# Kernel tuning notes

Hardware: AMD Instinct MI355X
Metric: run time of the kernel (lower is better)

The kernel has to match this reference:

```python
import jax, jax.numpy as jnp
import numpy as np

FEATURES = 768

def setup_inputs() -> dict:
    key = jax.random.key(0)
    k1, k2, kq, kd, kc = jax.random.split(key, 5)
    B, S1, S2 = 8, 2048, 2048
    bound = 1.0 / np.sqrt(FEATURES)  # nn.Linear default init range
    return {
        "matrix1": jax.random.normal(k1, (B, S1, FEATURES), dtype=jnp.float32),
        "matrix2": jax.random.normal(k2, (B, S2, FEATURES), dtype=jnp.float32),
        "w_q": jax.random.uniform(kq, (FEATURES,), jnp.float32, -bound, bound),
        "w_d": jax.random.uniform(kd, (FEATURES,), jnp.float32, -bound, bound),
        "w_c": jax.random.uniform(kc, (FEATURES,), jnp.float32, -bound, bound),
    }

def reference(matrix1, matrix2, w_q, w_d, w_c):
    # S[b,j,k] = (m1 @ w_q)[b,j] + (m2 @ w_d)[b,k] + sum_f w_c[f]*m1[b,j,f]*m2[b,k,f]
    Q = jnp.einsum('bjf,f->bj', matrix1, w_q)                # [B, S1]
    D = jnp.einsum('bkf,f->bk', matrix2, w_d)                # [B, S2]
    C = jnp.einsum('bjf,bkf->bjk', matrix1 * w_c, matrix2)   # [B, S1, S2]
    return Q[:, :, None] + D[:, None, :] + C
```

## Files before the change

kernel.cpp:

```cpp
#include <hip/hip_runtime.h>
#include <hip/hip_bf16.h>

#define S1 2048
#define S2 2048
#define FEAT 768
#define NB 8
#define BK 64
#define NKT (FEAT / BK)

typedef __attribute__((ext_vector_type(8))) short bf16x8;
typedef __attribute__((ext_vector_type(4))) float f32x4;
typedef __attribute__((ext_vector_type(4))) unsigned short us4;
typedef __attribute__((address_space(1))) const unsigned int gu32;
typedef __attribute__((address_space(3))) unsigned int lu32;

static __device__ __forceinline__ unsigned short f2bf(float x) {
    unsigned u = __builtin_bit_cast(unsigned, x);
    unsigned r = u + 0x7FFFu + ((u >> 16) & 1u);
    return (unsigned short)(r >> 16);
}

__global__ __launch_bounds__(256) void conv_kernel(
    const float* __restrict__ m1, const float* __restrict__ m2,
    const float* __restrict__ wq, const float* __restrict__ wd,
    const float* __restrict__ wc,
    unsigned short* __restrict__ A, unsigned short* __restrict__ Bm,
    float* __restrict__ Q, float* __restrict__ D) {
    int wave = threadIdx.x >> 6;
    int lane = threadIdx.x & 63;
    int g = blockIdx.x * 4 + wave;
    bool isA = (g < NB * S1);
    int row = isA ? g : g - NB * S1;
    const float* src = isA ? m1 : m2;
    const float* w   = isA ? wq : wd;
    unsigned short* dst = (isA ? A : Bm) + (size_t)row * FEAT;
    const float4* rp = (const float4*)(src + (size_t)row * FEAT);
    const float4* wp = (const float4*)w;
    const float4* cp = (const float4*)wc;
    float acc = 0.f;
#pragma unroll
    for (int i = 0; i < 3; ++i) {
        int idx = lane + 64 * i;
        float4 a = rp[idx];
        float4 b = wp[idx];
        acc += a.x * b.x + a.y * b.y + a.z * b.z + a.w * b.w;
        float4 c;
        if (isA) c = cp[idx]; else c = float4{1.f, 1.f, 1.f, 1.f};
        us4 v = { f2bf(a.x * c.x), f2bf(a.y * c.y),
                  f2bf(a.z * c.z), f2bf(a.w * c.w) };
        *(us4*)(dst + idx * 4) = v;
    }
#pragma unroll
    for (int s = 32; s; s >>= 1) acc += __shfl_xor(acc, s, 64);
    if (lane == 0) (isA ? Q : D)[row] = acc;
}

__global__ __launch_bounds__(256, 3) void gemm128_kernel(
    const unsigned short* __restrict__ A, const unsigned short* __restrict__ Bm,
    const float* __restrict__ Q, const float* __restrict__ D,
    float* __restrict__ out) {

    __shared__ __align__(16) char sA[128 * 128];
    __shared__ __align__(16) char sB[128 * 128];

    const int bid = blockIdx.x;
    const int b   = bid & 7;
    const int idx = bid >> 3;
    const int qd  = idx >> 6;
    const int w64 = idx & 63;
    const int tm  = ((qd >> 1) << 3) | (w64 >> 3);
    const int tn  = ((qd & 1) << 3) | (w64 & 7);

    const int tid  = threadIdx.x;
    const int lane = tid & 63;
    const int wave = tid >> 6;
    const int wm = wave >> 1, wn = wave & 1;

    const char* Ab = (const char*)(A + ((size_t)b * S1 + (size_t)tm * 128) * FEAT);
    const char* Bb = (const char*)(Bm + ((size_t)b * S2 + (size_t)tn * 128) * FEAT);

    const int srow = lane >> 3;
    const int scol = ((lane & 7) ^ (srow & 7)) * 16;

    const int fr = lane & 15;
    const int kg = lane >> 4;

    f32x4 acc[4][4];
#pragma unroll
    for (int m = 0; m < 4; ++m)
#pragma unroll
        for (int n = 0; n < 4; ++n) acc[m][n] = (f32x4)0.f;

    for (int kt = 0; kt < NKT; ++kt) {
        __syncthreads();
#pragma unroll
        for (int i = 0; i < 4; ++i) {
            const int rb = wave * 32 + i * 8;
            __builtin_amdgcn_global_load_lds(
                (gu32*)(Ab + (size_t)(rb + srow) * (FEAT * 2) + kt * (BK * 2) + scol),
                (lu32*)(sA + rb * 128), 16, 0, 0);
            __builtin_amdgcn_global_load_lds(
                (gu32*)(Bb + (size_t)(rb + srow) * (FEAT * 2) + kt * (BK * 2) + scol),
                (lu32*)(sB + rb * 128), 16, 0, 0);
        }
        __syncthreads();

#pragma unroll
        for (int s = 0; s < 2; ++s) {
            bf16x8 af[4], bfr[4];
#pragma unroll
            for (int m = 0; m < 4; ++m) {
                int r = wm * 64 + m * 16 + fr;
                int coff = (s * 64 + kg * 16) ^ ((r & 7) << 4);
                af[m] = *(const bf16x8*)(sA + r * 128 + coff);
            }
#pragma unroll
            for (int n = 0; n < 4; ++n) {
                int r = wn * 64 + n * 16 + fr;
                int coff = (s * 64 + kg * 16) ^ ((r & 7) << 4);
                bfr[n] = *(const bf16x8*)(sB + r * 128 + coff);
            }
#pragma unroll
            for (int m = 0; m < 4; ++m)
#pragma unroll
                for (int n = 0; n < 4; ++n)
                    acc[m][n] = __builtin_amdgcn_mfma_f32_16x16x32_bf16(
                        af[m], bfr[n], acc[m][n], 0, 0, 0);
        }
    }

    const float* Qb = Q + b * S1 + tm * 128;
    const float* Db = D + b * S2 + tn * 128;
    float dv[4];
#pragma unroll
    for (int n = 0; n < 4; ++n) dv[n] = Db[wn * 64 + n * 16 + fr];

    const size_t outbase = ((size_t)b * S1 + (size_t)tm * 128) * S2 + (size_t)tn * 128;
#pragma unroll
    for (int m = 0; m < 4; ++m) {
#pragma unroll
        for (int i = 0; i < 4; ++i) {
            int rl = wm * 64 + m * 16 + kg * 4 + i;
            float qv = Qb[rl];
            float* orow = out + outbase + (size_t)rl * S2 + wn * 64;
#pragma unroll
            for (int n = 0; n < 4; ++n)
                orow[n * 16 + fr] = acc[m][n][i] + qv + dv[n];
        }
    }
}

__global__ __launch_bounds__(256) void qd_kernel(
    const float* __restrict__ m1, const float* __restrict__ m2,
    const float* __restrict__ wq, const float* __restrict__ wd,
    float* __restrict__ Q, float* __restrict__ D) {
    int wave = threadIdx.x >> 6;
    int lane = threadIdx.x & 63;
    int g = blockIdx.x * 4 + wave;
    const float* src; const float* w; float* dst; int row;
    if (g < NB * S1) { src = m1; w = wq; dst = Q; row = g; }
    else             { src = m2; w = wd; dst = D; row = g - NB * S1; }
    const float4* rp = (const float4*)(src + (size_t)row * FEAT);
    const float4* wp = (const float4*)w;
    float acc = 0.f;
#pragma unroll
    for (int i = 0; i < 3; ++i) {
        float4 a = rp[lane + 64 * i];
        float4 b = wp[lane + 64 * i];
        acc += a.x * b.x + a.y * b.y + a.z * b.z + a.w * b.w;
    }
#pragma unroll
    for (int s = 32; s; s >>= 1) acc += __shfl_xor(acc, s, 64);
    if (lane == 0) dst[row] = acc;
}

__global__ __launch_bounds__(256) void gemm_kernel(
    const float* __restrict__ m1, const float* __restrict__ m2,
    const float* __restrict__ wc,
    const float* __restrict__ Q, const float* __restrict__ D,
    float* __restrict__ out) {

    __shared__ __align__(16) char sA[128 * 64 * 2];
    __shared__ __align__(16) char sB[128 * 64 * 2];
    __shared__ float wcs[FEAT];

    const int tid = threadIdx.x;
    const int blk = blockIdx.x;
    const int b  = blk >> 8;
    const int t  = blk & 255;
    const int tm = t >> 4, tn = t & 15;

    for (int i = tid; i < FEAT; i += 256) wcs[i] = wc[i];

    const float* Abase = m1 + ((size_t)b * S1 + (size_t)tm * 128) * FEAT;
    const float* Bbase = m2 + ((size_t)b * S2 + (size_t)tn * 128) * FEAT;

    const int lane = tid & 63;
    const int wave = tid >> 6;
    const int wm = wave >> 1, wn = wave & 1;

    f32x4 acc[4][4];
#pragma unroll
    for (int m = 0; m < 4; ++m)
#pragma unroll
        for (int n = 0; n < 4; ++n) acc[m][n] = (f32x4)0.f;

    const int col4 = tid & 15;
    const int row0 = tid >> 4;

    __syncthreads();

    for (int ks = 0; ks < FEAT / 64; ++ks) {
        float4 wc4 = *(const float4*)&wcs[ks * 64 + col4 * 4];
        const float4* Ak = (const float4*)(Abase + ks * 64);
        const float4* Bk = (const float4*)(Bbase + ks * 64);

        __syncthreads();
#pragma unroll
        for (int i = 0; i < 8; ++i) {
            int r = row0 + 16 * i;
            float4 a = Ak[(size_t)r * (FEAT / 4) + col4];
            us4 av = { f2bf(a.x * wc4.x), f2bf(a.y * wc4.y),
                       f2bf(a.z * wc4.z), f2bf(a.w * wc4.w) };
            int off = r * 128 + ((col4 * 8) ^ ((r & 7) << 4));
            *(us4*)(sA + off) = av;
        }
#pragma unroll
        for (int i = 0; i < 8; ++i) {
            int r = row0 + 16 * i;
            float4 v = Bk[(size_t)r * (FEAT / 4) + col4];
            us4 bv = { f2bf(v.x), f2bf(v.y), f2bf(v.z), f2bf(v.w) };
            int off = r * 128 + ((col4 * 8) ^ ((r & 7) << 4));
            *(us4*)(sB + off) = bv;
        }
        __syncthreads();

#pragma unroll
        for (int s = 0; s < 2; ++s) {
            bf16x8 af[4], bfr[4];
#pragma unroll
            for (int m = 0; m < 4; ++m) {
                int r = wm * 64 + m * 16 + (lane & 15);
                int coff = (s * 64 + (lane >> 4) * 16) ^ ((r & 7) << 4);
                af[m] = *(const bf16x8*)(sA + r * 128 + coff);
            }
#pragma unroll
            for (int n = 0; n < 4; ++n) {
                int r = wn * 64 + n * 16 + (lane & 15);
                int coff = (s * 64 + (lane >> 4) * 16) ^ ((r & 7) << 4);
                bfr[n] = *(const bf16x8*)(sB + r * 128 + coff);
            }
#pragma unroll
            for (int m = 0; m < 4; ++m)
#pragma unroll
                for (int n = 0; n < 4; ++n)
                    acc[m][n] = __builtin_amdgcn_mfma_f32_16x16x32_bf16(
                        af[m], bfr[n], acc[m][n], 0, 0, 0);
        }
    }

    const float* Qb = Q + b * S1 + tm * 128;
    const float* Db = D + b * S2 + tn * 128;
    float dv[4];
#pragma unroll
    for (int n = 0; n < 4; ++n) dv[n] = Db[wn * 64 + n * 16 + (lane & 15)];

    const size_t outbase = ((size_t)b * S1 + (size_t)tm * 128) * S2 + (size_t)tn * 128;
#pragma unroll
    for (int m = 0; m < 4; ++m) {
#pragma unroll
        for (int i = 0; i < 4; ++i) {
            int rl = wm * 64 + m * 16 + (lane >> 4) * 4 + i;
            float qv = Qb[rl];
            float* orow = out + outbase + (size_t)rl * S2 + wn * 64;
#pragma unroll
            for (int n = 0; n < 4; ++n) {
                int cl = n * 16 + (lane & 15);
                orow[cl] = acc[m][n][i] + qv + dv[n];
            }
        }
    }
}

extern "C" void kernel_launch(void* const* d_in, const int* in_sizes, int n_in,
                              void* d_out, int out_size, void* d_ws, size_t ws_size,
                              hipStream_t stream) {
    const float* m1 = (const float*)d_in[0];
    const float* m2 = (const float*)d_in[1];
    const float* wq = (const float*)d_in[2];
    const float* wd = (const float*)d_in[3];
    const float* wc = (const float*)d_in[4];
    float* out = (float*)d_out;

    const size_t elems = (size_t)NB * S1 * FEAT;
    const size_t need = 2 * elems * sizeof(unsigned short)
                      + (size_t)(NB * S1 + NB * S2) * sizeof(float);

    if (ws_size >= need) {
        unsigned short* Abuf = (unsigned short*)d_ws;
        unsigned short* Bbuf = Abuf + elems;
        float* Q  = (float*)(Bbuf + elems);
        float* Dv = Q + NB * S1;
        conv_kernel<<<(NB * S1 + NB * S2) / 4, 256, 0, stream>>>(
            m1, m2, wq, wd, wc, Abuf, Bbuf, Q, Dv);
        gemm128_kernel<<<NB * 16 * 16, 256, 0, stream>>>(Abuf, Bbuf, Q, Dv, out);
    } else {
        float* Q  = (float*)d_ws;
        float* Dv = Q + NB * S1;
        qd_kernel<<<(2 * NB * S1) / 4, 256, 0, stream>>>(m1, m2, wq, wd, Q, Dv);
        gemm_kernel<<<NB * 256, 256, 0, stream>>>(m1, m2, wc, Q, Dv, out);
    }
}
```

Measured before the change: 88.30 us.

## Double-buffer LDS tiles with BK=32 to overlap global loads with MFMA

Reworks the bf16 GEMM main loop to use two LDS buffers with half-width K tiles. The next tile is prefetched via global_load_lds while MFMAs run on the current one, and the two barriers per iteration become a single waitcnt plus barrier. The LDS swizzle is changed to match the 64-byte row stride, and the occupancy hint rises from 3 to 4 blocks. The cost is twice as many loop iterations with less MFMA work between barriers.

```diff
diff --git a/kernel.cpp b/kernel.cpp
--- a/kernel.cpp
+++ b/kernel.cpp
@@ -5,7 +5,7 @@
 #define S2 2048
 #define FEAT 768
 #define NB 8
-#define BK 64
+#define BK 32
 #define NKT (FEAT / BK)
 
 typedef __attribute__((ext_vector_type(8))) short bf16x8;
@@ -55,13 +55,12 @@
     if (lane == 0) (isA ? Q : D)[row] = acc;
 }
 
-__global__ __launch_bounds__(256, 3) void gemm128_kernel(
+__global__ __launch_bounds__(256, 4) void gemm128p_kernel(
     const unsigned short* __restrict__ A, const unsigned short* __restrict__ Bm,
     const float* __restrict__ Q, const float* __restrict__ D,
     float* __restrict__ out) {
 
-    __shared__ __align__(16) char sA[128 * 128];
-    __shared__ __align__(16) char sB[128 * 128];
+    __shared__ __align__(16) char ldsb[2 * 16384];
 
     const int bid = blockIdx.x;
     const int b   = bid & 7;
@@ -79,56 +78,70 @@
     const char* Ab = (const char*)(A + ((size_t)b * S1 + (size_t)tm * 128) * FEAT);
     const char* Bb = (const char*)(Bm + ((size_t)b * S2 + (size_t)tn * 128) * FEAT);
 
-    const int srow = lane >> 3;
-    const int scol = ((lane & 7) ^ (srow & 7)) * 16;
-
-    const int fr = lane & 15;
+    const int srow   = lane >> 2;
+    const int scolsw = (((lane & 3) ^ ((lane >> 3) & 3)) * 16);
+
+    const int fr  = lane & 15;
+    const int fkb = (((lane >> 4) ^ ((lane >> 1) & 3)) * 16);
+
+    f32x4 acc[4][4];
+#pragma unroll
+    for (int m = 0; m < 4; ++m)
+#pragma unroll
+        for (int n = 0; n < 4; ++n) acc[m][n] = (f32x4)0.f;
+
+#define STAGE(kt) do {                                                            \
+    char* _buf = ldsb + ((kt) & 1) * 16384;                                       \
+    _Pragma("unroll")                                                             \
+    for (int _i = 0; _i < 2; ++_i) {                                              \
+        const int _j = wave * 2 + _i;            \
+        __builtin_amdgcn_global_load_lds(                                         \
+            (gu32*)(Ab + (size_t)(_j * 16 + srow) * (FEAT * 2)                    \
+                       + (kt) * (BK * 2) + scolsw),                               \
+            (lu32*)(_buf + _j * 1024), 16, 0, 0);                                 \
+        __builtin_amdgcn_global_load_lds(                                         \
+            (gu32*)(Bb + (size_t)(_j * 16 + srow) * (FEAT * 2)                    \
+                       + (kt) * (BK * 2) + scolsw),                               \
+            (lu32*)(_buf + 8192 + _j * 1024), 16, 0, 0);                          \
+    }                                                                             \
+} while (0)
+
+    STAGE(0);
+    asm volatile("s_waitcnt vmcnt(0)" ::: "memory");
+    __builtin_amdgcn_s_barrier();
+    asm volatile("" ::: "memory");
+
+#pragma unroll 2
+    for (int kt = 0; kt < NKT; ++kt) {
+        if (kt + 1 < NKT) STAGE(kt + 1);
+
+        const char* bufc = ldsb + (kt & 1) * 16384;
+        bf16x8 af[4], bfr[4];
+#pragma unroll
+        for (int n = 0; n < 4; ++n) {
+            int r = wn * 64 + n * 16 + fr;
+            bfr[n] = *(const bf16x8*)(bufc + 8192 + r * 64 + fkb);
+        }
+#pragma unroll
+        for (int m = 0; m < 4; ++m) {
+            int r = wm * 64 + m * 16 + fr;
+            af[m] = *(const bf16x8*)(bufc + r * 64 + fkb);
+        }
+#pragma unroll
+        for (int m = 0; m < 4; ++m)
+#pragma unroll
+            for (int n = 0; n < 4; ++n)
+                acc[m][n] = __builtin_amdgcn_mfma_f32_16x16x32_bf16(
+                    af[m], bfr[n], acc[m][n], 0, 0, 0);
+
+        if (kt + 1 < NKT) {
+            asm volatile("s_waitcnt vmcnt(0)" ::: "memory");
+            __builtin_amdgcn_s_barrier();
+            asm volatile("" ::: "memory");
+        }
+    }
+
     const int kg = lane >> 4;
-
-    f32x4 acc[4][4];
-#pragma unroll
-    for (int m = 0; m < 4; ++m)
-#pragma unroll
-        for (int n = 0; n < 4; ++n) acc[m][n] = (f32x4)0.f;
-
-    for (int kt = 0; kt < NKT; ++kt) {
-        __syncthreads();
-#pragma unroll
-        for (int i = 0; i < 4; ++i) {
-            const int rb = wave * 32 + i * 8;
-            __builtin_amdgcn_global_load_lds(
-                (gu32*)(Ab + (size_t)(rb + srow) * (FEAT * 2) + kt * (BK * 2) + scol),
-                (lu32*)(sA + rb * 128), 16, 0, 0);
-            __builtin_amdgcn_global_load_lds(
-                (gu32*)(Bb + (size_t)(rb + srow) * (FEAT * 2) + kt * (BK * 2) + scol),
-                (lu32*)(sB + rb * 128), 16, 0, 0);
-        }
-        __syncthreads();
-
-#pragma unroll
-        for (int s = 0; s < 2; ++s) {
-            bf16x8 af[4], bfr[4];
-#pragma unroll
-            for (int m = 0; m < 4; ++m) {
-                int r = wm * 64 + m * 16 + fr;
-                int coff = (s * 64 + kg * 16) ^ ((r & 7) << 4);
-                af[m] = *(const bf16x8*)(sA + r * 128 + coff);
-            }
-#pragma unroll
-            for (int n = 0; n < 4; ++n) {
-                int r = wn * 64 + n * 16 + fr;
-                int coff = (s * 64 + kg * 16) ^ ((r & 7) << 4);
-                bfr[n] = *(const bf16x8*)(sB + r * 128 + coff);
-            }
-#pragma unroll
-            for (int m = 0; m < 4; ++m)
-#pragma unroll
-                for (int n = 0; n < 4; ++n)
-                    acc[m][n] = __builtin_amdgcn_mfma_f32_16x16x32_bf16(
-                        af[m], bfr[n], acc[m][n], 0, 0, 0);
-        }
-    }
-
     const float* Qb = Q + b * S1 + tm * 128;
     const float* Db = D + b * S2 + tn * 128;
     float dv[4];
@@ -148,6 +161,7 @@
                 orow[n * 16 + fr] = acc[m][n][i] + qv + dv[n];
         }
     }
+#undef STAGE
 }
 
 __global__ __launch_bounds__(256) void qd_kernel(
@@ -303,7 +317,7 @@
         float* Dv = Q + NB * S1;
         conv_kernel<<<(NB * S1 + NB * S2) / 4, 256, 0, stream>>>(
             m1, m2, wq, wd, wc, Abuf, Bbuf, Q, Dv);
-        gemm128_kernel<<<NB * 16 * 16, 256, 0, stream>>>(Abuf, Bbuf, Q, Dv, out);
+        gemm128p_kernel<<<NB * 16 * 16, 256, 0, stream>>>(Abuf, Bbuf, Q, Dv, out);
     } else {
         float* Q  = (float*)d_ws;
         float* Dv = Q + NB * S1;
```

Measured after the change: 98.47 us. 11.5% more time.

## Load GEMM fragments directly from global memory instead of LDS staging

Applied to the files above, without the earlier changes.

The bf16 GEMM no longer stages A and B tiles through shared memory with barriers. Each wave reads its MFMA operand fragments straight from global memory in a fully unrolled K loop, and occupancy is raised to 4 blocks per CU. This removes LDS traffic and __syncthreads overhead. In exchange it relies on L1/L2 caching for operand reuse across waves and issues strided 16-byte global loads.

```diff
diff --git a/kernel.cpp b/kernel.cpp
--- a/kernel.cpp
+++ b/kernel.cpp
@@ -5,14 +5,12 @@
 #define S2 2048
 #define FEAT 768
 #define NB 8
-#define BK 64
+#define BK 32
 #define NKT (FEAT / BK)
 
 typedef __attribute__((ext_vector_type(8))) short bf16x8;
 typedef __attribute__((ext_vector_type(4))) float f32x4;
 typedef __attribute__((ext_vector_type(4))) unsigned short us4;
-typedef __attribute__((address_space(1))) const unsigned int gu32;
-typedef __attribute__((address_space(3))) unsigned int lu32;
 
 static __device__ __forceinline__ unsigned short f2bf(float x) {
     unsigned u = __builtin_bit_cast(unsigned, x);
@@ -55,13 +53,10 @@
     if (lane == 0) (isA ? Q : D)[row] = acc;
 }
 
-__global__ __launch_bounds__(256, 3) void gemm128_kernel(
+__global__ __launch_bounds__(256, 4) void gemm128g_kernel(
     const unsigned short* __restrict__ A, const unsigned short* __restrict__ Bm,
     const float* __restrict__ Q, const float* __restrict__ D,
     float* __restrict__ out) {
-
-    __shared__ __align__(16) char sA[128 * 128];
-    __shared__ __align__(16) char sB[128 * 128];
 
     const int bid = blockIdx.x;
     const int b   = bid & 7;
@@ -76,57 +71,35 @@
     const int wave = tid >> 6;
     const int wm = wave >> 1, wn = wave & 1;
 
-    const char* Ab = (const char*)(A + ((size_t)b * S1 + (size_t)tm * 128) * FEAT);
-    const char* Bb = (const char*)(Bm + ((size_t)b * S2 + (size_t)tn * 128) * FEAT);
-
-    const int srow = lane >> 3;
-    const int scol = ((lane & 7) ^ (srow & 7)) * 16;
-
     const int fr = lane & 15;
     const int kg = lane >> 4;
 
+    const char* Arow = (const char*)(A + ((size_t)b * S1 + (size_t)tm * 128
+                                          + wm * 64 + fr) * FEAT) + kg * 16;
+    const char* Brow = (const char*)(Bm + ((size_t)b * S2 + (size_t)tn * 128
+                                          + wn * 64 + fr) * FEAT) + kg * 16;
+
     f32x4 acc[4][4];
 #pragma unroll
     for (int m = 0; m < 4; ++m)
 #pragma unroll
         for (int n = 0; n < 4; ++n) acc[m][n] = (f32x4)0.f;
 
+#pragma unroll
     for (int kt = 0; kt < NKT; ++kt) {
-        __syncthreads();
-#pragma unroll
-        for (int i = 0; i < 4; ++i) {
-            const int rb = wave * 32 + i * 8;
-            __builtin_amdgcn_global_load_lds(
-                (gu32*)(Ab + (size_t)(rb + srow) * (FEAT * 2) + kt * (BK * 2) + scol),
-                (lu32*)(sA + rb * 128), 16, 0, 0);
-            __builtin_amdgcn_global_load_lds(
-                (gu32*)(Bb + (size_t)(rb + srow) * (FEAT * 2) + kt * (BK * 2) + scol),
-                (lu32*)(sB + rb * 128), 16, 0, 0);
-        }
-        __syncthreads();
-
-#pragma unroll
-        for (int s = 0; s < 2; ++s) {
-            bf16x8 af[4], bfr[4];
-#pragma unroll
-            for (int m = 0; m < 4; ++m) {
-                int r = wm * 64 + m * 16 + fr;
-                int coff = (s * 64 + kg * 16) ^ ((r & 7) << 4);
-                af[m] = *(const bf16x8*)(sA + r * 128 + coff);
-            }
-#pragma unroll
-            for (int n = 0; n < 4; ++n) {
-                int r = wn * 64 + n * 16 + fr;
-                int coff = (s * 64 + kg * 16) ^ ((r & 7) << 4);
-                bfr[n] = *(const bf16x8*)(sB + r * 128 + coff);
-            }
-#pragma unroll
-            for (int m = 0; m < 4; ++m)
-#pragma unroll
-                for (int n = 0; n < 4; ++n)
-                    acc[m][n] = __builtin_amdgcn_mfma_f32_16x16x32_bf16(
-                        af[m], bfr[n], acc[m][n], 0, 0, 0);
-        }
+        bf16x8 af[4], bf[4];
+#pragma unroll
+        for (int m = 0; m < 4; ++m)
+            af[m] = *(const bf16x8*)(Arow + (size_t)m * (16 * FEAT * 2) + kt * 64);
+#pragma unroll
+        for (int n = 0; n < 4; ++n)
+            bf[n] = *(const bf16x8*)(Brow + (size_t)n * (16 * FEAT * 2) + kt * 64);
+#pragma unroll
+        for (int m = 0; m < 4; ++m)
+#pragma unroll
+            for (int n = 0; n < 4; ++n)
+                acc[m][n] = __builtin_amdgcn_mfma_f32_16x16x32_bf16(
+                    af[m], bf[n], acc[m][n], 0, 0, 0);
     }
 
     const float* Qb = Q + b * S1 + tm * 128;
@@ -303,7 +276,7 @@
         float* Dv = Q + NB * S1;
         conv_kernel<<<(NB * S1 + NB * S2) / 4, 256, 0, stream>>>(
             m1, m2, wq, wd, wc, Abuf, Bbuf, Q, Dv);
-        gemm128_kernel<<<NB * 16 * 16, 256, 0, stream>>>(Abuf, Bbuf, Q, Dv, out);
+        gemm128g_kernel<<<NB * 16 * 16, 256, 0, stream>>>(Abuf, Bbuf, Q, Dv, out);
     } else {
         float* Q  = (float*)d_ws;
         float* Dv = Q + NB * S1;
```

After: 215.1 us. 144% more time.
